# Kernel optimization log

Hardware: AMD Instinct MI355X
Metric: run time of the kernel (lower is better)

Reference implementation:

```python
import jax, jax.numpy as jnp
import numpy as np

KEY_DIM = 64  # scaling uses key_dim, NOT the full projection dim (faithful to source)


def setup_inputs() -> dict:
    key = jax.random.key(0)
    ks = jax.random.split(key, 9)
    B, S, D = 4, 4096, 512
    P = 512  # heads * key_dim = 8 * 64
    s = 0.02
    return {
        "x": jax.random.normal(ks[0], (B, S, D), jnp.float32),
        "Wq": jax.random.normal(ks[1], (D, P), jnp.float32) * s,
        "bq": jnp.zeros((P,), jnp.float32),
        "Wk": jax.random.normal(ks[2], (D, P), jnp.float32) * s,
        "bk": jnp.zeros((P,), jnp.float32),
        "Wv": jax.random.normal(ks[3], (D, P), jnp.float32) * s,
        "bv": jnp.zeros((P,), jnp.float32),
        "Wo": jax.random.normal(ks[4], (P, D), jnp.float32) * s,
        "bo": jnp.zeros((D,), jnp.float32),
    }


def reference(x, Wq, bq, Wk, bk, Wv, bv, Wo, bo):
    # Manual QKV projections over the FULL heads*key_dim dim (no head split,
    # exactly as the original layer).
    q = jnp.einsum("bsd,dp->bsp", x, Wq) + bq
    k = jnp.einsum("bsd,dp->bsp", x, Wk) + bk
    v = jnp.einsum("bsd,dp->bsp", x, Wv) + bv
    scale = 1.0 / jnp.sqrt(jnp.float32(KEY_DIM))
    scores = jnp.einsum("bsp,btp->bst", q, k) * scale  # [B,S,S]
    attn = jax.nn.softmax(scores, axis=-1)
    attended = jnp.einsum("bst,btp->bsp", attn, v)
    return jnp.einsum("bsp,pd->bsd", attended, Wo) + bo
```

## Files before the change

### kernel.cpp

```cpp
#include <hip/hip_runtime.h>
#include <hip/hip_bf16.h>

typedef __bf16 bf16x8 __attribute__((ext_vector_type(8)));
typedef float  floatx4 __attribute__((ext_vector_type(4)));

#define MFMA16(a, b, c) __builtin_amdgcn_mfma_f32_16x16x32_bf16((a), (b), (c), 0, 0, 0)

static constexpr int BATCH = 4;
static constexpr int SEQ   = 4096;
static constexpr int MTOT  = BATCH * SEQ;

__device__ __forceinline__ void gload16(const void* gsrc, void* ldst)
{
    auto* g = reinterpret_cast<const __attribute__((address_space(1))) unsigned int*>(
        reinterpret_cast<unsigned long long>(gsrc));
    auto* l = reinterpret_cast<__attribute__((address_space(3))) unsigned int*>(
        reinterpret_cast<unsigned long long>(ldst));
    __builtin_amdgcn_global_load_lds(g, l, 16, 0, 0);
}

__global__ __launch_bounds__(256) void cvt_x(
    const float* __restrict__ x, __bf16* __restrict__ xb)
{
    const size_t i = ((size_t)blockIdx.x * 256 + threadIdx.x) * 8;
    const float4 a = *reinterpret_cast<const float4*>(x + i);
    const float4 c = *reinterpret_cast<const float4*>(x + i + 4);
    bf16x8 r;
    r[0] = (__bf16)a.x; r[1] = (__bf16)a.y; r[2] = (__bf16)a.z; r[3] = (__bf16)a.w;
    r[4] = (__bf16)c.x; r[5] = (__bf16)c.y; r[6] = (__bf16)c.z; r[7] = (__bf16)c.w;
    *reinterpret_cast<bf16x8*>(xb + i) = r;
}

__global__ __launch_bounds__(256) void transpose_w(
    const float* __restrict__ W, __bf16* __restrict__ WT)
{
    __shared__ __bf16 tile[64 * 68];
    const int t   = blockIdx.x;
    const int k0  = (t >> 3) * 64;
    const int n0  = (t & 7) * 64;
    const int tid = threadIdx.x;
#pragma unroll
    for (int it = 0; it < 4; ++it) {
        const int flat = it * 1024 + tid * 4;
        const int r = flat >> 6;
        const int c = flat & 63;
        const float4 v = *reinterpret_cast<const float4*>(
            W + (size_t)(k0 + r) * 512 + n0 + c);
        tile[r * 68 + c + 0] = (__bf16)v.x;
        tile[r * 68 + c + 1] = (__bf16)v.y;
        tile[r * 68 + c + 2] = (__bf16)v.z;
        tile[r * 68 + c + 3] = (__bf16)v.w;
    }
    __syncthreads();
#pragma unroll
    for (int it = 0; it < 2; ++it) {
        const int gid = it * 256 + tid;
        const int n  = gid >> 3;
        const int k8 = (gid & 7) * 8;
        bf16x8 r8;
#pragma unroll
        for (int j = 0; j < 8; ++j) r8[j] = tile[(k8 + j) * 68 + n];
        *reinterpret_cast<bf16x8*>(WT + (size_t)(n0 + n) * 512 + k0 + k8) = r8;
    }
}

__global__ __launch_bounds__(256, 2) void qkv_gemm(
    const __bf16* __restrict__ xb,
    const __bf16* __restrict__ WqT, const float* __restrict__ bq,
    const __bf16* __restrict__ WkT, const float* __restrict__ bk,
    const __bf16* __restrict__ WvT, const float* __restrict__ bv,
    __bf16* __restrict__ qb, __bf16* __restrict__ kb, __bf16* __restrict__ vbT)
{
    __shared__ __attribute__((aligned(16))) __bf16 As[64 * 64];
    __shared__ __attribute__((aligned(16))) __bf16 Bq[64 * 64];
    __shared__ __attribute__((aligned(16))) __bf16 Bk[64 * 64];
    __shared__ __attribute__((aligned(16))) __bf16 Bv[64 * 64];
    __shared__ __bf16 Cs[64 * 80];

    const int tid  = threadIdx.x;
    const int w    = tid >> 6;
    const int lane = tid & 63;
    const int quad = lane >> 4;
    const int l15  = lane & 15;
    const int fid  = blockIdx.x;
    const int n0   = (fid & 7) * 64;
    const int m0   = (fid >> 3) * 64;

    const int srow0 = w * 8 + (lane >> 3);
    const int sgrp  = lane & 7;

    floatx4 aq[4], ak[4], av[4];
#pragma unroll
    for (int nt = 0; nt < 4; ++nt) {
        aq[nt] = floatx4{0.f, 0.f, 0.f, 0.f};
        ak[nt] = floatx4{0.f, 0.f, 0.f, 0.f};
        av[nt] = floatx4{0.f, 0.f, 0.f, 0.f};
    }

    for (int k0 = 0; k0 < 512; k0 += 64) {
#pragma unroll
        for (int i = 0; i < 2; ++i) {
            const int r  = i * 32 + srow0;
            const int cg = (sgrp ^ (r & 7)) << 3;
            const int db = (i * 32 + w * 8) * 64;
            gload16(xb  + (size_t)(m0 + r) * 512 + k0 + cg, &As[db]);
            gload16(WqT + (size_t)(n0 + r) * 512 + k0 + cg, &Bq[db]);
            gload16(WkT + (size_t)(n0 + r) * 512 + k0 + cg, &Bk[db]);
            gload16(WvT + (size_t)(n0 + r) * 512 + k0 + cg, &Bv[db]);
        }
        __syncthreads();

#pragma unroll
        for (int kk = 0; kk < 2; ++kk) {
            const int arow = w * 16 + l15;
            const bf16x8 af = *reinterpret_cast<const bf16x8*>(
                &As[arow * 64 + (((kk * 4 + quad) ^ (arow & 7)) << 3)]);
#pragma unroll
            for (int nt = 0; nt < 4; ++nt) {
                const int brow = nt * 16 + l15;
                const int off  = brow * 64 + (((kk * 4 + quad) ^ (brow & 7)) << 3);
                aq[nt] = MFMA16(af, *reinterpret_cast<const bf16x8*>(&Bq[off]), aq[nt]);
                ak[nt] = MFMA16(af, *reinterpret_cast<const bf16x8*>(&Bk[off]), ak[nt]);
                av[nt] = MFMA16(af, *reinterpret_cast<const bf16x8*>(&Bv[off]), av[nt]);
            }
        }
        __syncthreads();
    }

#pragma unroll
    for (int nt = 0; nt < 4; ++nt) {
        const int col = n0 + nt * 16 + l15;
        const float bqv = bq[col], bkv = bk[col], bvv = bv[col];
#pragma unroll
        for (int r = 0; r < 4; ++r) {
            const int row = m0 + w * 16 + quad * 4 + r;
            qb[(size_t)row * 512 + col] = (__bf16)((aq[nt][r] + bqv) * 0.125f);
            kb[(size_t)row * 512 + col] = (__bf16)(ak[nt][r] + bkv);
            Cs[(nt * 16 + l15) * 80 + w * 16 + quad * 4 + r] = (__bf16)(av[nt][r] + bvv);
        }
    }
    __syncthreads();
    {
        const int bb = m0 >> 12;
        const int tb = m0 & 4095;
        __bf16* yb = vbT + (size_t)bb * 512 * 4096;
#pragma unroll
        for (int it = 0; it < 2; ++it) {
            const int flat = it * 2048 + tid * 8;
            const int pl = flat >> 6;
            const int c  = flat & 63;
            const bf16x8 vv = *reinterpret_cast<const bf16x8*>(&Cs[pl * 80 + c]);
            *reinterpret_cast<bf16x8*>(&yb[(size_t)(n0 + pl) * 4096 + tb + c]) = vv;
        }
    }
}

__global__ __launch_bounds__(256, 2) void out_gemm(
    const __bf16* __restrict__ A, const __bf16* __restrict__ WT,
    const float* __restrict__ bias, float* __restrict__ Y)
{
    __shared__ __attribute__((aligned(16))) __bf16 As[64 * 64];
    __shared__ __attribute__((aligned(16))) __bf16 Bs[64 * 64];

    const int tid  = threadIdx.x;
    const int w    = tid >> 6;
    const int lane = tid & 63;
    const int quad = lane >> 4;
    const int l15  = lane & 15;
    const int fid  = blockIdx.x;
    const int n0   = (fid & 7) * 64;
    const int m0   = (fid >> 3) * 64;

    const int srow0 = w * 8 + (lane >> 3);
    const int sgrp  = lane & 7;

    floatx4 acc[4];
#pragma unroll
    for (int nt = 0; nt < 4; ++nt) acc[nt] = floatx4{0.f, 0.f, 0.f, 0.f};

    for (int k0 = 0; k0 < 512; k0 += 64) {
#pragma unroll
        for (int i = 0; i < 2; ++i) {
            const int r  = i * 32 + srow0;
            const int cg = (sgrp ^ (r & 7)) << 3;
            const int db = (i * 32 + w * 8) * 64;
            gload16(A  + (size_t)(m0 + r) * 512 + k0 + cg, &As[db]);
            gload16(WT + (size_t)(n0 + r) * 512 + k0 + cg, &Bs[db]);
        }
        __syncthreads();

#pragma unroll
        for (int kk = 0; kk < 2; ++kk) {
            const int arow = w * 16 + l15;
            const bf16x8 af = *reinterpret_cast<const bf16x8*>(
                &As[arow * 64 + (((kk * 4 + quad) ^ (arow & 7)) << 3)]);
#pragma unroll
            for (int nt = 0; nt < 4; ++nt) {
                const int brow = nt * 16 + l15;
                const bf16x8 bfv = *reinterpret_cast<const bf16x8*>(
                    &Bs[brow * 64 + (((kk * 4 + quad) ^ (brow & 7)) << 3)]);
                acc[nt] = MFMA16(af, bfv, acc[nt]);
            }
        }
        __syncthreads();
    }

#pragma unroll
    for (int nt = 0; nt < 4; ++nt) {
        const int col = n0 + nt * 16 + l15;
        const float bv = bias[col];
#pragma unroll
        for (int r = 0; r < 4; ++r) {
            const int row = m0 + w * 16 + quad * 4 + r;
            Y[(size_t)row * 512 + col] = acc[nt][r] + bv;
        }
    }
}

__global__ __launch_bounds__(512, 2) void flash_attn(
    const __bf16* __restrict__ q, const __bf16* __restrict__ k,
    const __bf16* __restrict__ vT, __bf16* __restrict__ pO,
    float* __restrict__ lP)
{
    __shared__ __bf16 Kt[32 * 520];
    __shared__ __bf16 Vt[512 * 32];
    __shared__ __bf16 Pl[8 * 16 * 40];

    const int tid  = threadIdx.x;
    const int w    = tid >> 6;
    const int lane = tid & 63;
    const int quad = lane >> 4;
    const int l15  = lane & 15;

    const int fid = blockIdx.x;
    const int g   = fid & 7;
    const int hb  = g & 1;
    const int b   = g >> 1;
    const int q0  = (fid >> 3) * 128;
    const size_t boff = (size_t)b * SEQ * 512;

    bf16x8 qf[16];
    {
        const __bf16* qrow = q + boff + (size_t)(q0 + w * 16 + l15) * 512;
#pragma unroll
        for (int kk = 0; kk < 16; ++kk)
            qf[kk] = *reinterpret_cast<const bf16x8*>(qrow + kk * 32 + quad * 8);
    }

    floatx4 o[32];
#pragma unroll
    for (int i = 0; i < 32; ++i) o[i] = floatx4{0.f, 0.f, 0.f, 0.f};
    float lsum[4] = {0.f, 0.f, 0.f, 0.f};

    const __bf16* kB  = k + boff;
    const __bf16* vTb = vT + boff;
    const int tstart = hb * 2048;
    const int tend   = tstart + 2048;

    const int vprow = lane >> 2;
    const int vkoff = (((lane & 3) ^ ((lane >> 3) & 3)) << 3);

    {
        const __bf16* kbase = kB + (size_t)(tstart + w * 4) * 512 + lane * 8;
#pragma unroll
        for (int j = 0; j < 4; ++j)
            gload16(kbase + (size_t)j * 512, &Kt[(w * 4 + j) * 520]);
#pragma unroll
        for (int j = 0; j < 4; ++j) {
            const int p0 = (w * 4 + j) * 16;
            gload16(vTb + (size_t)(p0 + vprow) * 4096 + tstart + vkoff, &Vt[p0 * 32]);
        }
    }

    for (int t0 = tstart; t0 < tend; t0 += 32) {
        const int tn = (t0 + 32 < tend) ? t0 + 32 : t0;

        asm volatile("s_waitcnt vmcnt(4)" ::: "memory");
        __builtin_amdgcn_s_barrier();

        floatx4 sa0 = floatx4{0.f, 0.f, 0.f, 0.f};
        floatx4 sa1 = floatx4{0.f, 0.f, 0.f, 0.f};
        __builtin_amdgcn_s_setprio(1);
#pragma unroll
        for (int kk = 0; kk < 16; ++kk) {
            const bf16x8 kf0 = *reinterpret_cast<const bf16x8*>(
                &Kt[l15 * 520 + kk * 32 + quad * 8]);
            const bf16x8 kf1 = *reinterpret_cast<const bf16x8*>(
                &Kt[(16 + l15) * 520 + kk * 32 + quad * 8]);
            sa0 = MFMA16(qf[kk], kf0, sa0);
            sa1 = MFMA16(qf[kk], kf1, sa1);
        }
        __builtin_amdgcn_s_setprio(0);

#pragma unroll
        for (int r = 0; r < 4; ++r) {
            const float p0 = __expf(sa0[r]);
            const float p1 = __expf(sa1[r]);
            lsum[r] += p0 + p1;
            Pl[(w * 16 + quad * 4 + r) * 40 + l15]      = (__bf16)p0;
            Pl[(w * 16 + quad * 4 + r) * 40 + 16 + l15] = (__bf16)p1;
        }

        __builtin_amdgcn_s_barrier();

        {
            const __bf16* kbase = kB + (size_t)(tn + w * 4) * 512 + lane * 8;
#pragma unroll
            for (int j = 0; j < 4; ++j)
                gload16(kbase + (size_t)j * 512, &Kt[(w * 4 + j) * 520]);
        }

        asm volatile("s_waitcnt vmcnt(4)" ::: "memory");
        __builtin_amdgcn_s_barrier();

        const bf16x8 pf = *reinterpret_cast<const bf16x8*>(
            &Pl[(w * 16 + l15) * 40 + quad * 8]);
        const int vsw = ((quad ^ ((l15 >> 1) & 3)) << 3);
        __builtin_amdgcn_s_setprio(1);
#pragma unroll
        for (int pt = 0; pt < 32; ++pt) {
            const bf16x8 vf = *reinterpret_cast<const bf16x8*>(
                &Vt[(pt * 16 + l15) * 32 + vsw]);
            o[pt] = MFMA16(pf, vf, o[pt]);
        }
        __builtin_amdgcn_s_setprio(0);

        __builtin_amdgcn_s_barrier();

#pragma unroll
        for (int j = 0; j < 4; ++j) {
            const int p0 = (w * 4 + j) * 16;
            gload16(vTb + (size_t)(p0 + vprow) * 4096 + tn + vkoff, &Vt[p0 * 32]);
        }
    }
    asm volatile("s_waitcnt vmcnt(0)" ::: "memory");

#pragma unroll
    for (int r = 0; r < 4; ++r) {
#pragma unroll
        for (int off = 1; off < 16; off <<= 1)
            lsum[r] += __shfl_xor(lsum[r], off);
    }
    const int rowbase = b * SEQ + q0 + w * 16 + quad * 4;
    if (l15 == 0) {
#pragma unroll
        for (int r = 0; r < 4; ++r)
            lP[(size_t)hb * MTOT + rowbase + r] = lsum[r];
    }
    __bf16* pOh = pO + (size_t)hb * MTOT * 512;
#pragma unroll
    for (int pt = 0; pt < 32; ++pt) {
#pragma unroll
        for (int r = 0; r < 4; ++r)
            pOh[(size_t)(rowbase + r) * 512 + pt * 16 + l15] = (__bf16)o[pt][r];
    }
}

__global__ __launch_bounds__(256) void merge_attn(
    const __bf16* __restrict__ pO, const float* __restrict__ lP,
    __bf16* __restrict__ att)
{
    const int gidx = blockIdx.x * 256 + threadIdx.x;
    const int row  = gidx >> 6;
    const int c8   = (gidx & 63) * 8;
    const float li = 1.0f / (lP[row] + lP[MTOT + row]);
    const bf16x8 a = *reinterpret_cast<const bf16x8*>(&pO[(size_t)row * 512 + c8]);
    const bf16x8 bvv = *reinterpret_cast<const bf16x8*>(
        &pO[((size_t)MTOT + row) * 512 + c8]);
    bf16x8 r8;
#pragma unroll
    for (int j = 0; j < 8; ++j)
        r8[j] = (__bf16)(((float)a[j] + (float)bvv[j]) * li);
    *reinterpret_cast<bf16x8*>(&att[(size_t)row * 512 + c8]) = r8;
}

extern "C" void kernel_launch(void* const* d_in, const int* in_sizes, int n_in,
                              void* d_out, int out_size, void* d_ws, size_t ws_size,
                              hipStream_t stream)
{
    (void)in_sizes; (void)n_in; (void)out_size; (void)ws_size;

    const float* x  = (const float*)d_in[0];
    const float* Wq = (const float*)d_in[1];
    const float* bq = (const float*)d_in[2];
    const float* Wk = (const float*)d_in[3];
    const float* bk = (const float*)d_in[4];
    const float* Wv = (const float*)d_in[5];
    const float* bv = (const float*)d_in[6];
    const float* Wo = (const float*)d_in[7];
    const float* bo = (const float*)d_in[8];
    float* out = (float*)d_out;

    __bf16* qb  = (__bf16*)d_ws;
    __bf16* kb  = qb  + (size_t)MTOT * 512;
    __bf16* vbT = kb  + (size_t)MTOT * 512;
    float*  lP  = (float*)(vbT + (size_t)MTOT * 512);
    __bf16* pO  = (__bf16*)d_out;
    __bf16* ab  = qb;

    __bf16* xb  = (__bf16*)d_out;
    __bf16* WqT = xb  + (size_t)MTOT * 512;
    __bf16* WkT = WqT + 512 * 512;
    __bf16* WvT = WkT + 512 * 512;
    __bf16* WoT = kb;

    cvt_x<<<MTOT * 512 / 2048, 256, 0, stream>>>(x, xb);
    transpose_w<<<64, 256, 0, stream>>>(Wq, WqT);
    transpose_w<<<64, 256, 0, stream>>>(Wk, WkT);
    transpose_w<<<64, 256, 0, stream>>>(Wv, WvT);

    qkv_gemm<<<2048, 256, 0, stream>>>(xb, WqT, bq, WkT, bk, WvT, bv, qb, kb, vbT);

    flash_attn<<<256, 512, 0, stream>>>(qb, kb, vbT, pO, lP);

    transpose_w<<<64, 256, 0, stream>>>(Wo, WoT);
    merge_attn<<<MTOT * 64 / 256, 256, 0, stream>>>(pO, lP, ab);

    out_gemm<<<2048, 256, 0, stream>>>(ab, WoT, bo, out);
}
```

Baseline: 340.2 us.

## Repartition PV matmul by head-dim columns and stage output through LDS

The P·V step is reassigned so each wave owns a 64-column slice of the 512-wide head dim across all 128 query rows. It keeps four V fragments in registers and reads P fragments from shared memory, where before each wave read all 32 V fragments for its own 16 rows. This cuts LDS traffic for V per wave, at the cost of every wave reading all waves' P tiles, which requires an lgkmcnt wait before the barrier. The partial output is transposed through a shared buffer and written with coalesced 16-byte stores instead of scattered 2-byte stores.

Measured after the change: 348.0 us. +2.3%, slower.

```diff
diff --git a/kernel.cpp b/kernel.cpp
--- a/kernel.cpp
+++ b/kernel.cpp
@@ -222,9 +222,10 @@
     const __bf16* __restrict__ vT, __bf16* __restrict__ pO,
     float* __restrict__ lP)
 {
-    __shared__ __bf16 Kt[32 * 520];
-    __shared__ __bf16 Vt[512 * 32];
-    __shared__ __bf16 Pl[8 * 16 * 40];
+    __shared__ __attribute__((aligned(16))) __bf16 SH[38144];
+    __bf16* Kt = SH;
+    __bf16* Vt = SH + 16640;
+    __bf16* Pl = SH + 33024;
 
     const int tid  = threadIdx.x;
     const int w    = tid >> 6;
@@ -259,6 +260,7 @@
 
     const int vprow = lane >> 2;
     const int vkoff = (((lane & 3) ^ ((lane >> 3) & 3)) << 3);
+    const int vsw   = ((quad ^ ((l15 >> 1) & 3)) << 3);
 
     {
         const __bf16* kbase = kB + (size_t)(tstart + w * 4) * 512 + lane * 8;
@@ -301,6 +303,7 @@
             Pl[(w * 16 + quad * 4 + r) * 40 + 16 + l15] = (__bf16)p1;
         }
 
+        asm volatile("s_waitcnt lgkmcnt(0)" ::: "memory");
         __builtin_amdgcn_s_barrier();
 
         {
@@ -313,15 +316,20 @@
         asm volatile("s_waitcnt vmcnt(4)" ::: "memory");
         __builtin_amdgcn_s_barrier();
 
-        const bf16x8 pf = *reinterpret_cast<const bf16x8*>(
-            &Pl[(w * 16 + l15) * 40 + quad * 8]);
-        const int vsw = ((quad ^ ((l15 >> 1) & 3)) << 3);
+        bf16x8 vfr[4];
+#pragma unroll
+        for (int pb = 0; pb < 4; ++pb)
+            vfr[pb] = *reinterpret_cast<const bf16x8*>(
+                &Vt[((w * 4 + pb) * 16 + l15) * 32 + vsw]);
+
         __builtin_amdgcn_s_setprio(1);
 #pragma unroll
-        for (int pt = 0; pt < 32; ++pt) {
-            const bf16x8 vf = *reinterpret_cast<const bf16x8*>(
-                &Vt[(pt * 16 + l15) * 32 + vsw]);
-            o[pt] = MFMA16(pf, vf, o[pt]);
+        for (int rb = 0; rb < 8; ++rb) {
+            const bf16x8 pf = *reinterpret_cast<const bf16x8*>(
+                &Pl[(rb * 16 + l15) * 40 + quad * 8]);
+#pragma unroll
+            for (int pb = 0; pb < 4; ++pb)
+                o[pb * 8 + rb] = MFMA16(vfr[pb], pf, o[pb * 8 + rb]);
         }
         __builtin_amdgcn_s_setprio(0);
 
@@ -341,18 +349,41 @@
         for (int off = 1; off < 16; off <<= 1)
             lsum[r] += __shfl_xor(lsum[r], off);
     }
-    const int rowbase = b * SEQ + q0 + w * 16 + quad * 4;
+    const int lrowbase = b * SEQ + q0 + w * 16 + quad * 4;
     if (l15 == 0) {
 #pragma unroll
         for (int r = 0; r < 4; ++r)
-            lP[(size_t)hb * MTOT + rowbase + r] = lsum[r];
-    }
+            lP[(size_t)hb * MTOT + lrowbase + r] = lsum[r];
+    }
+
+    __bf16* Ot = SH;
     __bf16* pOh = pO + (size_t)hb * MTOT * 512;
-#pragma unroll
-    for (int pt = 0; pt < 32; ++pt) {
-#pragma unroll
-        for (int r = 0; r < 4; ++r)
-            pOh[(size_t)(rowbase + r) * 512 + pt * 16 + l15] = (__bf16)o[pt][r];
+    const int prowbase = b * SEQ + q0;
+#pragma unroll
+    for (int hh = 0; hh < 2; ++hh) {
+        __builtin_amdgcn_s_barrier();
+#pragma unroll
+        for (int rb2 = 0; rb2 < 4; ++rb2) {
+            const int rb = hh * 4 + rb2;
+#pragma unroll
+            for (int pb = 0; pb < 4; ++pb) {
+#pragma unroll
+                for (int r = 0; r < 4; ++r)
+                    Ot[(rb2 * 16 + l15) * 520 + (w * 4 + pb) * 16 + quad * 4 + r] =
+                        (__bf16)o[pb * 8 + rb][r];
+            }
+        }
+        asm volatile("s_waitcnt lgkmcnt(0)" ::: "memory");
+        __builtin_amdgcn_s_barrier();
+#pragma unroll
+        for (int it = 0; it < 8; ++it) {
+            const int id  = it * 512 + tid;
+            const int row = id >> 6;
+            const int c8  = (id & 63) * 8;
+            *reinterpret_cast<bf16x8*>(
+                pOh + (size_t)(prowbase + hh * 64 + row) * 512 + c8) =
+                *reinterpret_cast<const bf16x8*>(&Ot[row * 520 + c8]);
+        }
     }
 }
 
```
